# Optimization experiments

Measured on AMD Instinct MI355X. Metric: run time of the kernel, lower is better.

The kernel has to match this reference:

```python
import jax, jax.numpy as jnp
import numpy as np

B, S, D, H, G = 16, 512, 1024, 128, 256  # batch, seq, lstm_in, lstm_hidden, gat_dim

def _linear(x, W, b):
    return x @ W.T + b

def _lstm_dir(xs, Wih, Whh, bih, bhh, reverse):
    # xs: [S, B, Din] -> hs: [S, B, H]; PyTorch gate order i, f, g, o
    b = bih + bhh
    def step(carry, xt):
        h, c = carry
        z = xt @ Wih.T + h @ Whh.T + b
        i, f, g, o = jnp.split(z, 4, axis=-1)
        c = jax.nn.sigmoid(f) * c + jax.nn.sigmoid(i) * jnp.tanh(g)
        h = jax.nn.sigmoid(o) * jnp.tanh(c)
        return (h, c), h
    init = (jnp.zeros((xs.shape[1], Whh.shape[1]), xs.dtype),
            jnp.zeros((xs.shape[1], Whh.shape[1]), xs.dtype))
    _, hs = jax.lax.scan(step, init, xs, reverse=reverse)
    return hs

def _forward(x, adj,
             l0f_Wih, l0f_Whh, l0f_bih, l0f_bhh, l0b_Wih, l0b_Whh, l0b_bih, l0b_bhh,
             l1f_Wih, l1f_Whh, l1f_bih, l1f_bhh, l1b_Wih, l1b_Whh, l1b_bih, l1b_bhh,
             fc1_W, fc1_b, wattn_W, wattn_b, lin0_W, lin0_b, lin1_W, lin1_b,
             linf_W, linf_b, fcA_W, fcA_b, fcB_W, fcB_b, fcC_W, fcC_b):
    # ---- 2-layer bidirectional LSTM ----
    xs = jnp.swapaxes(x, 0, 1)  # [S, B, D]
    h0 = jnp.concatenate([_lstm_dir(xs, l0f_Wih, l0f_Whh, l0f_bih, l0f_bhh, False),
                          _lstm_dir(xs, l0b_Wih, l0b_Whh, l0b_bih, l0b_bhh, True)], axis=-1)
    h1 = jnp.concatenate([_lstm_dir(h0, l1f_Wih, l1f_Whh, l1f_bih, l1f_bhh, False),
                          _lstm_dir(h0, l1b_Wih, l1b_Whh, l1b_bih, l1b_bhh, True)], axis=-1)
    out_lstm = jnp.swapaxes(h1, 0, 1)  # [B, S, 2H]
    # ---- GAT on fc1(x) ----
    g = _linear(x, fc1_W, fc1_b)  # [B, S, G]
    idx = jnp.arange(S)
    adj = adj.at[:, idx, idx].set(1.0)
    eye = 1e-05 * jnp.eye(S, dtype=x.dtype)
    for l in range(4):
        g0 = g
        q = _linear(g, wattn_W[l], wattn_b[l])
        a = jax.nn.sigmoid(jnp.einsum('bij,bkj->bik', q, g)) + eye
        a = a * adj
        a = a / jnp.sum(a, axis=2, keepdims=True)
        g = jnp.einsum('bij,bjd->bid', a, g)
        g = jax.nn.relu(_linear(g, lin0_W[l], lin0_b[l]))
        g = jax.nn.relu(_linear(g, lin1_W[l], lin1_b[l]))
        g = g + g0
    g = _linear(g, linf_W, linf_b)
    # ---- head (dropout in eval mode -> identity) ----
    hidden = jnp.mean(jnp.concatenate([out_lstm, g], axis=2), axis=1)  # [B, 512]
    y = jax.nn.leaky_relu(_linear(hidden, fcA_W, fcA_b), 0.1)
    y = jax.nn.leaky_relu(_linear(y, fcB_W, fcB_b), 0.1)
    y = _linear(y, fcC_W, fcC_b)  # [B, 2]
    return y, hidden


def setup_inputs() -> dict:
    key = jax.random.key(0)
    ks = jax.random.split(key, 40)
    r = lambda k, shape: jax.random.normal(k, shape, jnp.float32) * 0.05
    inp = {}
    inp['x'] = jax.random.normal(ks[0], (B, S, D), jnp.float32)
    inp['adj'] = (jax.random.uniform(ks[1], (B, S, S)) < 0.05).astype(jnp.float32)
    # LSTM params: layer0 input D, layer1 input 2H; forward/backward directions
    inp['l0f_Wih'] = r(ks[2], (4 * H, D)); inp['l0f_Whh'] = r(ks[3], (4 * H, H))
    inp['l0f_bih'] = r(ks[4], (4 * H,));  inp['l0f_bhh'] = r(ks[5], (4 * H,))
    inp['l0b_Wih'] = r(ks[6], (4 * H, D)); inp['l0b_Whh'] = r(ks[7], (4 * H, H))
    inp['l0b_bih'] = r(ks[8], (4 * H,));  inp['l0b_bhh'] = r(ks[9], (4 * H,))
    inp['l1f_Wih'] = r(ks[10], (4 * H, 2 * H)); inp['l1f_Whh'] = r(ks[11], (4 * H, H))
    inp['l1f_bih'] = r(ks[12], (4 * H,)); inp['l1f_bhh'] = r(ks[13], (4 * H,))
    inp['l1b_Wih'] = r(ks[14], (4 * H, 2 * H)); inp['l1b_Whh'] = r(ks[15], (4 * H, H))
    inp['l1b_bih'] = r(ks[16], (4 * H,)); inp['l1b_bhh'] = r(ks[17], (4 * H,))
    inp['fc1_W'] = r(ks[18], (G, D)); inp['fc1_b'] = r(ks[19], (G,))
    inp['wattn_W'] = r(ks[20], (4, G, G)); inp['wattn_b'] = r(ks[21], (4, G))
    inp['lin0_W'] = r(ks[22], (4, G, G)); inp['lin0_b'] = r(ks[23], (4, G))
    inp['lin1_W'] = r(ks[24], (4, G, G)); inp['lin1_b'] = r(ks[25], (4, G))
    inp['linf_W'] = r(ks[26], (G, G)); inp['linf_b'] = r(ks[27], (G,))
    inp['fcA_W'] = r(ks[28], (128, 512)); inp['fcA_b'] = r(ks[29], (128,))
    inp['fcB_W'] = r(ks[30], (32, 128)); inp['fcB_b'] = r(ks[31], (32,))
    inp['fcC_W'] = r(ks[32], (2, 32)); inp['fcC_b'] = r(ks[33], (2,))
    return inp


def reference(x, adj,
              l0f_Wih, l0f_Whh, l0f_bih, l0f_bhh, l0b_Wih, l0b_Whh, l0b_bih, l0b_bhh,
              l1f_Wih, l1f_Whh, l1f_bih, l1f_bhh, l1b_Wih, l1b_Whh, l1b_bih, l1b_bhh,
              fc1_W, fc1_b, wattn_W, wattn_b, lin0_W, lin0_b, lin1_W, lin1_b,
              linf_W, linf_b, fcA_W, fcA_b, fcB_W, fcB_b, fcC_W, fcC_b):
    return _forward(x, adj,
                    l0f_Wih, l0f_Whh, l0f_bih, l0f_bhh, l0b_Wih, l0b_Whh, l0b_bih, l0b_bhh,
                    l1f_Wih, l1f_Whh, l1f_bih, l1f_bhh, l1b_Wih, l1b_Whh, l1b_bih, l1b_bhh,
                    fc1_W, fc1_b, wattn_W, wattn_b, lin0_W, lin0_b, lin1_W, lin1_b,
                    linf_W, linf_b, fcA_W, fcA_b, fcB_W, fcB_b, fcC_W, fcC_b)
```

## Files before the change

kernel.cpp:

```cpp
#include <hip/hip_runtime.h>
#include <stdint.h>

#define B_ 16
#define S_ 512
#define D_ 1024
#define H4 512
#define G_ 256

typedef unsigned short u16;
using short8 = __attribute__((ext_vector_type(8))) short;
using f32x4  = __attribute__((ext_vector_type(4))) float;

__device__ __forceinline__ u16 f2bf(float f){
  unsigned int u = __float_as_uint(f);
  u += 0x7fffu + ((u >> 16) & 1u);
  return (u16)(u >> 16);
}
__device__ __forceinline__ float bf2f(u16 h){
  return __uint_as_float(((unsigned int)h) << 16);
}

struct CvtSegs {
  const float4* src[14];
  short4* dst[14];
  int blk0[15];
};
__global__ __launch_bounds__(256) void cvt_multi(CvtSegs cs){
  int blk = blockIdx.x;
  int s = 0;
  #pragma unroll
  for (int k = 0; k < 14; ++k) if (cs.blk0[k + 1] <= blk) s = k + 1;
  int i = (blk - cs.blk0[s]) * 256 + threadIdx.x;
  float4 v = cs.src[s][i];
  short4 o;
  o.x = (short)f2bf(v.x); o.y = (short)f2bf(v.y);
  o.z = (short)f2bf(v.z); o.w = (short)f2bf(v.w);
  cs.dst[s][i] = o;
}

__global__ __launch_bounds__(256) void bias_prep(const float* a,const float* b,const float* c,const float* d,
                                                 const float* e,const float* f,const float* g,const float* h,
                                                 float* out){
  int i = blockIdx.x * 256 + threadIdx.x;
  if (i >= 2048) return;
  int p = i >> 9, k = i & 511;
  const float* x1 = (p==0)?a:(p==1)?c:(p==2)?e:g;
  const float* x2 = (p==0)?b:(p==1)?d:(p==2)?f:h;
  out[i] = x1[k] + x2[k];
}

template<int EPI, bool OUT_BF16, int PERM, bool RESID>
__device__ __forceinline__ void gemm_bt_body(
    const u16* __restrict__ A, const u16* __restrict__ W,
    const float* __restrict__ bias, const u16* __restrict__ resid,
    const float* __restrict__ ex,
    void* __restrict__ outp, int M, int N, int K,
    long sA, long sW, long sO, int bx, int by, int bz)
{
  const u16* Ab = A + (long)bz * sA;
  const u16* Wb = W + (long)bz * sW;
  const int bm0 = by * 64, bn0 = bx * 64;
  const int tid = threadIdx.x;
  const int l = tid & 63, wid = tid >> 6;
  const int wm = (wid >> 1) * 32, wn = (wid & 1) * 32;
  const int lr = l & 15, lk8 = (l >> 4) * 8;

  const f32x4 z4 = {0.f, 0.f, 0.f, 0.f};
  f32x4 acc[2][2] = {{z4, z4}, {z4, z4}};

  const u16* Ap0 = Ab + (long)(bm0 + wm + lr) * K + lk8;
  const u16* Wp0 = Wb + (long)(bn0 + wn + lr) * K + lk8;
  for (int k0 = 0; k0 < K; k0 += 32) {
    short8 a0 = *reinterpret_cast<const short8*>(Ap0 + k0);
    short8 a1 = *reinterpret_cast<const short8*>(Ap0 + (long)16 * K + k0);
    short8 b0 = *reinterpret_cast<const short8*>(Wp0 + k0);
    short8 b1 = *reinterpret_cast<const short8*>(Wp0 + (long)16 * K + k0);
    acc[0][0] = __builtin_amdgcn_mfma_f32_16x16x32_bf16(a0, b0, acc[0][0], 0, 0, 0);
    acc[0][1] = __builtin_amdgcn_mfma_f32_16x16x32_bf16(a0, b1, acc[0][1], 0, 0, 0);
    acc[1][0] = __builtin_amdgcn_mfma_f32_16x16x32_bf16(a1, b0, acc[1][0], 0, 0, 0);
    acc[1][1] = __builtin_amdgcn_mfma_f32_16x16x32_bf16(a1, b1, acc[1][1], 0, 0, 0);
  }
  #pragma unroll
  for (int mt = 0; mt < 2; ++mt)
  #pragma unroll
  for (int nt = 0; nt < 2; ++nt) {
    int n = bn0 + wn + 16 * nt + lr;
    float bv = bias ? bias[n] : 0.f;
    #pragma unroll
    for (int r = 0; r < 4; ++r) {
      int m = bm0 + wm + 16 * mt + (l >> 4) * 4 + r;
      float v = acc[mt][nt][r] + bv;
      if (EPI == 1) v = fmaxf(v, 0.f);
      if (EPI == 2) {
        float sg = __fdividef(1.f, 1.f + __expf(-v));
        v = (n == m) ? (sg + 1e-5f) : sg * ex[((long)bz * 512 + m) * 512 + n];
      }
      if (EPI == 3) v *= ex[(long)bz * 512 + m];
      if (RESID) v += bf2f(resid[(long)m * N + n]);
      long oi;
      if (PERM == 2) {
        int t = m & 511, b = m >> 9;
        oi = (long)((t * 16 + b) * 128 + (n & 127)) * 4 + (n >> 7);
      } else {
        oi = (long)bz * sO + (long)m * N + n;
      }
      if (OUT_BF16) ((u16*)outp)[oi] = f2bf(v);
      else          ((float*)outp)[oi] = v;
    }
  }
}

template<int EPI, bool OUT_BF16, int PERM, bool RESID>
__global__ __launch_bounds__(256) void gemm_bt(
    const u16* __restrict__ A, const u16* __restrict__ W,
    const float* __restrict__ bias, const u16* __restrict__ resid,
    const float* __restrict__ ex,
    void* __restrict__ outp, int M, int N, int K,
    long sA, long sW, long sO)
{
  gemm_bt_body<EPI, OUT_BF16, PERM, RESID>(A, W, bias, resid, ex, outp, M, N, K,
                                           sA, sW, sO, blockIdx.x, blockIdx.y, blockIdx.z);
}

__global__ __launch_bounds__(256) void proj2(
    const u16* __restrict__ A, const u16* __restrict__ W0, const u16* __restrict__ W1,
    const float* __restrict__ bias, float* __restrict__ O0, float* __restrict__ O1, int K)
{
  int z = blockIdx.z;
  gemm_bt_body<0, false, 2, false>(A, z ? W1 : W0, bias + z * 512, nullptr, nullptr,
                                   z ? O1 : O0, 8192, 512, K, 0, 0, 0,
                                   blockIdx.x, blockIdx.y, 0);
}

__device__ __forceinline__ void gemm_bt_body8(
    const u16* __restrict__ A, const u16* __restrict__ W,
    const float* __restrict__ bias, u16* __restrict__ out,
    int N, int K, int bx, int by)
{
  const int bm0 = by * 64, bn0 = bx * 128;
  const int tid = threadIdx.x;
  const int l = tid & 63, wid = tid >> 6;
  const int wm = (wid >> 2) * 32, wn = (wid & 3) * 32;
  const int lr = l & 15, lk8 = (l >> 4) * 8;

  const f32x4 z4 = {0.f, 0.f, 0.f, 0.f};
  f32x4 acc[2][2] = {{z4, z4}, {z4, z4}};

  const u16* Ap0 = A + (long)(bm0 + wm + lr) * K + lk8;
  const u16* Wp0 = W + (long)(bn0 + wn + lr) * K + lk8;
  for (int k0 = 0; k0 < K; k0 += 32) {
    short8 a0 = *reinterpret_cast<const short8*>(Ap0 + k0);
    short8 a1 = *reinterpret_cast<const short8*>(Ap0 + (long)16 * K + k0);
    short8 b0 = *reinterpret_cast<const short8*>(Wp0 + k0);
    short8 b1 = *reinterpret_cast<const short8*>(Wp0 + (long)16 * K + k0);
    acc[0][0] = __builtin_amdgcn_mfma_f32_16x16x32_bf16(a0, b0, acc[0][0], 0, 0, 0);
    acc[0][1] = __builtin_amdgcn_mfma_f32_16x16x32_bf16(a0, b1, acc[0][1], 0, 0, 0);
    acc[1][0] = __builtin_amdgcn_mfma_f32_16x16x32_bf16(a1, b0, acc[1][0], 0, 0, 0);
    acc[1][1] = __builtin_amdgcn_mfma_f32_16x16x32_bf16(a1, b1, acc[1][1], 0, 0, 0);
  }
  #pragma unroll
  for (int mt = 0; mt < 2; ++mt)
  #pragma unroll
  for (int nt = 0; nt < 2; ++nt) {
    int n = bn0 + wn + 16 * nt + lr;
    float bv = bias[n];
    #pragma unroll
    for (int r = 0; r < 4; ++r) {
      int m = bm0 + wm + 16 * mt + (l >> 4) * 4 + r;
      out[(long)m * N + n] = f2bf(acc[mt][nt][r] + bv);
    }
  }
}

__device__ __forceinline__ void lstm_scan9_body(
    const float* __restrict__ X, const u16* __restrict__ Whh,
    u16* __restrict__ Hout, int dir, int bat0)
{
  __shared__ __align__(16) u16 hbuf[2][16][136];

  const int tid = threadIdx.x;
  const int l = tid & 63, w = tid >> 6;
  const int lr = l & 15, lk = l >> 4;

  short8 bfrag[4][4];
  #pragma unroll
  for (int g = 0; g < 4; ++g)
    #pragma unroll
    for (int ks = 0; ks < 4; ++ks)
      bfrag[g][ks] = *reinterpret_cast<const short8*>(
          Whh + (g * 128 + 16 * w + lr) * 128 + 32 * ks + 8 * lk);

  for (int i = tid; i < 2 * 16 * 136; i += 512) ((u16*)hbuf)[i] = 0;

  float c = 0.f;
  const f32x4 z4 = {0.f, 0.f, 0.f, 0.f};

  auto ldX = [&](int t) -> float4 {
    int ta = dir ? (S_ - 1 - t) : t;
    return *reinterpret_cast<const float4*>(
        X + (size_t)((ta * 16 + bat0 + lk) * 128 + 16 * w + lr) * 4);
  };
  float4 xA = ldX(0), xB = ldX(1), xC = ldX(2), xD;
  __syncthreads();

  auto step = [&](int t, float4& xc, float4& xt, int tload) {
    const int p = t & 1;
    short8 af[4];
    #pragma unroll
    for (int ks = 0; ks < 4; ++ks)
      af[ks] = *reinterpret_cast<const short8*>(&hbuf[p][lr][32 * ks + 8 * lk]);
    f32x4 acc[4] = {z4, z4, z4, z4};
    #pragma unroll
    for (int g = 0; g < 4; ++g)
      #pragma unroll
      for (int ks = 0; ks < 4; ++ks)
        acc[g] = __builtin_amdgcn_mfma_f32_16x16x32_bf16(af[ks], bfrag[g][ks], acc[g], 0, 0, 0);
    if (tload < S_) xt = ldX(tload);
    float zi = acc[0][0] + xc.x;
    float zf = acc[1][0] + xc.y;
    float zg = acc[2][0] + xc.z;
    float zo = acc[3][0] + xc.w;
    float si = __fdividef(1.f, 1.f + __expf(-zi));
    float sf = __fdividef(1.f, 1.f + __expf(-zf));
    float so = __fdividef(1.f, 1.f + __expf(-zo));
    float eg = __expf(2.f * zg);
    float tg = 1.f - __fdividef(2.f, eg + 1.f);
    c = sf * c + si * tg;
    float ec = __expf(2.f * c);
    float tc = 1.f - __fdividef(2.f, ec + 1.f);
    u16 hb = f2bf(so * tc);
    int ta = dir ? (S_ - 1 - t) : t;
    hbuf[p ^ 1][4 * lk][16 * w + lr] = hb;
    Hout[((size_t)(bat0 + lk) * S_ + ta) * 256 + dir * 128 + 16 * w + lr] = hb;
    asm volatile("s_waitcnt lgkmcnt(0)" ::: "memory");
    __builtin_amdgcn_s_barrier();
  };

  for (int t = 0; t < S_; t += 4) {
    step(t,     xA, xD, t + 3);
    step(t + 1, xB, xA, t + 4);
    step(t + 2, xC, xB, t + 5);
    step(t + 3, xD, xC, t + 6);
  }
}

__global__ __launch_bounds__(512, 1) void scan_fused(
    const float* __restrict__ Xf, const float* __restrict__ Xb,
    const u16* __restrict__ Whhf, const u16* __restrict__ Whhb,
    u16* __restrict__ Hout,
    const u16* __restrict__ gA, const u16* __restrict__ gW,
    const float* __restrict__ gb, u16* __restrict__ gOut, int gK)
{
  if (blockIdx.x < 8) {
    int dir = blockIdx.x & 1, bat0 = (blockIdx.x >> 1) * 4;
    lstm_scan9_body(dir ? Xb : Xf, dir ? Whhb : Whhf, Hout, dir, bat0);
  } else {
    int bi = blockIdx.x - 8;
    gemm_bt_body8(gA, gW, gb, gOut, 256, gK, bi & 1, bi >> 1);
  }
}

__device__ __forceinline__ void transpose_body(const u16* __restrict__ in, u16* __restrict__ out,
                                               int bz, int s0, int d0)
{
  __shared__ u16 tile[32][33];
  int tx = threadIdx.x & 31, ty = threadIdx.x >> 5;
  const u16* ip = in + (long)bz * 512 * 256;
  u16* op = out + (long)bz * 256 * 512;
  #pragma unroll
  for (int k = 0; k < 32; k += 8) tile[ty + k][tx] = ip[(long)(s0 + ty + k) * 256 + d0 + tx];
  __syncthreads();
  #pragma unroll
  for (int k = 0; k < 32; k += 8) op[(long)(d0 + ty + k) * 512 + s0 + tx] = tile[tx][ty + k];
}

__global__ __launch_bounds__(256) void transpose_g(const u16* __restrict__ in, u16* __restrict__ out)
{
  transpose_body(in, out, blockIdx.z, blockIdx.x * 32, blockIdx.y * 32);
}

__global__ __launch_bounds__(256) void wattn_trans(
    const u16* __restrict__ gcur, const u16* __restrict__ wW, const float* __restrict__ wb,
    u16* __restrict__ qb, u16* __restrict__ gT)
{
  if (blockIdx.x < 512) {
    int b = blockIdx.x;
    gemm_bt_body<0, true, 0, false>(gcur, wW, wb, nullptr, nullptr, qb,
                                    8192, 256, 256, 0, 0, 0, b & 3, b >> 2, 0);
  } else {
    int b = blockIdx.x - 512;
    int bz = b >> 7, rem = b & 127;
    transpose_body(gcur, gT, bz, (rem & 15) * 32, (rem >> 4) * 32);
  }
}

__global__ __launch_bounds__(256) void rowsum_inv(const u16* __restrict__ abf, float* __restrict__ rinv)
{
  int bz = blockIdx.y;
  int row = blockIdx.x * 4 + (threadIdx.x >> 6);
  int l = threadIdx.x & 63;
  short8 v = *reinterpret_cast<const short8*>(abf + ((size_t)bz * 512 + row) * 512 + l * 8);
  float s = 0.f;
  #pragma unroll
  for (int k = 0; k < 8; ++k) s += bf2f((u16)v[k]);
  #pragma unroll
  for (int off = 32; off; off >>= 1) s += __shfl_xor(s, off);
  if (l == 0) rinv[bz * 512 + row] = __fdividef(1.f, s);
}

__global__ __launch_bounds__(256) void mean_cat(
    const u16* __restrict__ lstm, const u16* __restrict__ gf, float* __restrict__ dout)
{
  int b = blockIdx.x;
  for (int cc = threadIdx.x; cc < 512; cc += 256) {
    const u16* src = (cc < 256) ? (lstm + (long)b * 512 * 256 + cc)
                                : (gf   + (long)b * 512 * 256 + (cc - 256));
    float s = 0.f;
    for (int t = 0; t < 512; ++t) s += bf2f(src[(long)t * 256]);
    dout[32 + b * 512 + cc] = s * (1.f / 512.f);
  }
}

__global__ __launch_bounds__(256) void head_kernel(
    const float* __restrict__ hidden,
    const float* __restrict__ fcA_W, const float* __restrict__ fcA_b,
    const float* __restrict__ fcB_W, const float* __restrict__ fcB_b,
    const float* __restrict__ fcC_W, const float* __restrict__ fcC_b,
    float* __restrict__ y)
{
  __shared__ float hb[16 * 512];
  __shared__ float ab[16 * 128];
  __shared__ float bb[16 * 32];
  int tid = threadIdx.x;
  for (int i = tid; i < 8192; i += 256) hb[i] = hidden[i];
  __syncthreads();
  for (int o = tid; o < 2048; o += 256) {
    int b = o >> 7, jj = o & 127;
    float acc = fcA_b[jj];
    const float* wrow = fcA_W + jj * 512;
    const float* hrow = hb + b * 512;
    for (int k = 0; k < 512; ++k) acc += hrow[k] * wrow[k];
    ab[o] = acc > 0.f ? acc : 0.1f * acc;
  }
  __syncthreads();
  for (int o = tid; o < 512; o += 256) {
    int b = o >> 5, jj = o & 31;
    float acc = fcB_b[jj];
    for (int k = 0; k < 128; ++k) acc += ab[b * 128 + k] * fcB_W[jj * 128 + k];
    bb[o] = acc > 0.f ? acc : 0.1f * acc;
  }
  __syncthreads();
  if (tid < 32) {
    int b = tid >> 1, jj = tid & 1;
    float acc = fcC_b[jj];
    for (int k = 0; k < 32; ++k) acc += bb[b * 32 + k] * fcC_W[jj * 32 + k];
    y[b * 2 + jj] = acc;
  }
}

extern "C" void kernel_launch(void* const* d_in, const int* in_sizes, int n_in,
                              void* d_out, int out_size, void* d_ws, size_t ws_size,
                              hipStream_t stream)
{
  const float* x       = (const float*)d_in[0];
  const float* adj     = (const float*)d_in[1];
  const float* l0f_Wih = (const float*)d_in[2];
  const float* l0f_Whh = (const float*)d_in[3];
  const float* l0f_bih = (const float*)d_in[4];
  const float* l0f_bhh = (const float*)d_in[5];
  const float* l0b_Wih = (const float*)d_in[6];
  const float* l0b_Whh = (const float*)d_in[7];
  const float* l0b_bih = (const float*)d_in[8];
  const float* l0b_bhh = (const float*)d_in[9];
  const float* l1f_Wih = (const float*)d_in[10];
  const float* l1f_Whh = (const float*)d_in[11];
  const float* l1f_bih = (const float*)d_in[12];
  const float* l1f_bhh = (const float*)d_in[13];
  const float* l1b_Wih = (const float*)d_in[14];
  const float* l1b_Whh = (const float*)d_in[15];
  const float* l1b_bih = (const float*)d_in[16];
  const float* l1b_bhh = (const float*)d_in[17];
  const float* fc1_W   = (const float*)d_in[18];
  const float* fc1_b   = (const float*)d_in[19];
  const float* wattn_W = (const float*)d_in[20];
  const float* wattn_b = (const float*)d_in[21];
  const float* lin0_W  = (const float*)d_in[22];
  const float* lin0_b  = (const float*)d_in[23];
  const float* lin1_W  = (const float*)d_in[24];
  const float* lin1_b  = (const float*)d_in[25];
  const float* linf_W  = (const float*)d_in[26];
  const float* linf_b  = (const float*)d_in[27];
  const float* fcA_W   = (const float*)d_in[28];
  const float* fcA_b   = (const float*)d_in[29];
  const float* fcB_W   = (const float*)d_in[30];
  const float* fcB_b   = (const float*)d_in[31];
  const float* fcC_W   = (const float*)d_in[32];
  const float* fcC_b   = (const float*)d_in[33];

  char* wp = (char*)d_ws;
  auto alloc = [&](size_t n) -> void* { void* p = wp; wp += (n + 255) & ~(size_t)255; return p; };

  u16* x_bf     = (u16*)alloc((size_t)B_ * S_ * D_ * 2);
  u16* w0f_ih   = (u16*)alloc((size_t)512 * 1024 * 2);
  u16* w0b_ih   = (u16*)alloc((size_t)512 * 1024 * 2);
  u16* w1f_ih   = (u16*)alloc((size_t)512 * 256 * 2);
  u16* w1b_ih   = (u16*)alloc((size_t)512 * 256 * 2);
  u16* w0f_hh   = (u16*)alloc((size_t)512 * 128 * 2);
  u16* w0b_hh   = (u16*)alloc((size_t)512 * 128 * 2);
  u16* w1f_hh   = (u16*)alloc((size_t)512 * 128 * 2);
  u16* w1b_hh   = (u16*)alloc((size_t)512 * 128 * 2);
  u16* wfc1     = (u16*)alloc((size_t)256 * 1024 * 2);
  u16* wattn_bf = (u16*)alloc((size_t)4 * 256 * 256 * 2);
  u16* wlin0_bf = (u16*)alloc((size_t)4 * 256 * 256 * 2);
  u16* wlin1_bf = (u16*)alloc((size_t)4 * 256 * 256 * 2);
  u16* wlinf_bf = (u16*)alloc((size_t)256 * 256 * 2);
  float* bias4  = (float*)alloc((size_t)2048 * 4);
  float* X0f    = (float*)alloc((size_t)S_ * 16 * 512 * 4);
  float* X0b    = (float*)alloc((size_t)S_ * 16 * 512 * 4);
  u16* h0       = (u16*)alloc((size_t)B_ * S_ * 256 * 2);
  u16* lstm_out = (u16*)alloc((size_t)B_ * S_ * 256 * 2);
  u16* gA       = (u16*)alloc((size_t)B_ * S_ * 256 * 2);
  u16* gB       = (u16*)alloc((size_t)B_ * S_ * 256 * 2);
  u16* qb       = (u16*)alloc((size_t)B_ * S_ * 256 * 2);
  u16* gT       = (u16*)alloc((size_t)B_ * S_ * 256 * 2);
  u16* t1       = (u16*)alloc((size_t)B_ * S_ * 256 * 2);
  u16* t2       = (u16*)alloc((size_t)B_ * S_ * 256 * 2);
  u16* abf      = (u16*)alloc((size_t)B_ * S_ * S_ * 2);
  float* rinv   = (float*)alloc((size_t)B_ * S_ * 4);

  CvtSegs cs;
  int nb = 0, si = 0;
  auto seg = [&](const float* s, u16* d, int n) {
    cs.src[si] = (const float4*)s; cs.dst[si] = (short4*)d;
    cs.blk0[si] = nb; nb += (n / 4 + 255) / 256; ++si;
  };
  seg(x, x_bf, B_ * S_ * D_);
  seg(l0f_Wih, w0f_ih, 512 * 1024);
  seg(l0b_Wih, w0b_ih, 512 * 1024);
  seg(l1f_Wih, w1f_ih, 512 * 256);
  seg(l1b_Wih, w1b_ih, 512 * 256);
  seg(l0f_Whh, w0f_hh, 512 * 128);
  seg(l0b_Whh, w0b_hh, 512 * 128);
  seg(l1f_Whh, w1f_hh, 512 * 128);
  seg(l1b_Whh, w1b_hh, 512 * 128);
  seg(fc1_W, wfc1, 256 * 1024);
  seg(wattn_W, wattn_bf, 4 * 256 * 256);
  seg(lin0_W, wlin0_bf, 4 * 256 * 256);
  seg(lin1_W, wlin1_bf, 4 * 256 * 256);
  seg(linf_W, wlinf_bf, 256 * 256);
  for (int k = si; k <= 14; ++k) cs.blk0[k] = nb;
  cvt_multi<<<nb, 256, 0, stream>>>(cs);
  bias_prep<<<8, 256, 0, stream>>>(l0f_bih, l0f_bhh, l0b_bih, l0b_bhh,
                                   l1f_bih, l1f_bhh, l1b_bih, l1b_bhh, bias4);

  proj2<<<dim3(8, 128, 2), 256, 0, stream>>>(x_bf, w0f_ih, w0b_ih, bias4, X0f, X0b, 1024);
  scan_fused<<<8 + 256, 512, 0, stream>>>(X0f, X0b, w0f_hh, w0b_hh, h0,
                                          x_bf, wfc1, fc1_b, gA, 1024);
  proj2<<<dim3(8, 128, 2), 256, 0, stream>>>(h0, w1f_ih, w1b_ih, bias4 + 1024, X0f, X0b, 256);
  scan_fused<<<8 + 256, 512, 0, stream>>>(X0f, X0b, w1f_hh, w1b_hh, lstm_out,
                                          gA, wattn_bf, wattn_b, qb, 256);

  u16* gcur = gA; u16* gnext = gB;
  for (int lyr = 0; lyr < 4; ++lyr) {
    if (lyr == 0)
      transpose_g<<<dim3(16, 8, 16), 256, 0, stream>>>(gcur, gT);
    else
      wattn_trans<<<512 + 2048, 256, 0, stream>>>(gcur, wattn_bf + lyr * 65536,
                                                  wattn_b + lyr * 256, qb, gT);
    gemm_bt<2, true, 0, false><<<dim3(8, 8, 16), 256, 0, stream>>>(
        qb, gcur, nullptr, nullptr, adj, abf, 512, 512, 256, 131072, 131072, 262144);
    rowsum_inv<<<dim3(128, 16), 256, 0, stream>>>(abf, rinv);
    gemm_bt<3, true, 0, false><<<dim3(4, 8, 16), 256, 0, stream>>>(
        abf, gT, nullptr, nullptr, rinv, t1, 512, 256, 512, 262144, 131072, 131072);
    gemm_bt<1, true, 0, false><<<dim3(4, 128, 1), 256, 0, stream>>>(
        t1, wlin0_bf + lyr * 65536, lin0_b + lyr * 256, nullptr, nullptr, t2, 8192, 256, 256, 0, 0, 0);
    gemm_bt<1, true, 0, true><<<dim3(4, 128, 1), 256, 0, stream>>>(
        t2, wlin1_bf + lyr * 65536, lin1_b + lyr * 256, gcur, nullptr, gnext, 8192, 256, 256, 0, 0, 0);
    u16* tmp = gcur; gcur = gnext; gnext = tmp;
  }
  gemm_bt<0, true, 0, false><<<dim3(4, 128, 1), 256, 0, stream>>>(
      gcur, wlinf_bf, linf_b, nullptr, nullptr, t2, 8192, 256, 256, 0, 0, 0);

  mean_cat<<<16, 256, 0, stream>>>(lstm_out, t2, (float*)d_out);
  head_kernel<<<1, 256, 0, stream>>>((const float*)d_out + 32,
                                     fcA_W, fcA_b, fcB_W, fcB_b, fcC_W, fcC_b,
                                     (float*)d_out);
}
```

Baseline: 1.225 ms.

## Run full GAT pipeline inside LSTM scan kernels with global-flag grid barriers

Moves the whole GAT stack (fc1, all four attention layers, and the final linear) into the two persistent scan kernels. Blocks beyond the eight LSTM blocks execute GAT stages, separated by atomic-counter grid barriers, so the GAT work overlaps the latency-bound recurrent scans instead of running as a chain of separate launches afterward. Each 512-thread block is treated as two virtual 256-thread workers. The risk is deadlock if the 264 blocks cannot all be resident at once, plus the cost of spin barriers. mean_cat is also rewritten so each thread sums one lstm column and one GAT column with coalesced reads.

```diff
diff --git a/kernel.cpp b/kernel.cpp
--- a/kernel.cpp
+++ b/kernel.cpp
@@ -55,12 +55,11 @@
     const float* __restrict__ bias, const u16* __restrict__ resid,
     const float* __restrict__ ex,
     void* __restrict__ outp, int M, int N, int K,
-    long sA, long sW, long sO, int bx, int by, int bz)
+    long sA, long sW, long sO, int bx, int by, int bz, int tid)
 {
   const u16* Ab = A + (long)bz * sA;
   const u16* Wb = W + (long)bz * sW;
   const int bm0 = by * 64, bn0 = bx * 64;
-  const int tid = threadIdx.x;
   const int l = tid & 63, wid = tid >> 6;
   const int wm = (wid >> 1) * 32, wn = (wid & 1) * 32;
   const int lr = l & 15, lk8 = (l >> 4) * 8;
@@ -110,18 +109,6 @@
   }
 }
 
-template<int EPI, bool OUT_BF16, int PERM, bool RESID>
-__global__ __launch_bounds__(256) void gemm_bt(
-    const u16* __restrict__ A, const u16* __restrict__ W,
-    const float* __restrict__ bias, const u16* __restrict__ resid,
-    const float* __restrict__ ex,
-    void* __restrict__ outp, int M, int N, int K,
-    long sA, long sW, long sO)
-{
-  gemm_bt_body<EPI, OUT_BF16, PERM, RESID>(A, W, bias, resid, ex, outp, M, N, K,
-                                           sA, sW, sO, blockIdx.x, blockIdx.y, blockIdx.z);
-}
-
 __global__ __launch_bounds__(256) void proj2(
     const u16* __restrict__ A, const u16* __restrict__ W0, const u16* __restrict__ W1,
     const float* __restrict__ bias, float* __restrict__ O0, float* __restrict__ O1, int K)
@@ -129,47 +116,36 @@
   int z = blockIdx.z;
   gemm_bt_body<0, false, 2, false>(A, z ? W1 : W0, bias + z * 512, nullptr, nullptr,
                                    z ? O1 : O0, 8192, 512, K, 0, 0, 0,
-                                   blockIdx.x, blockIdx.y, 0);
-}
-
-__device__ __forceinline__ void gemm_bt_body8(
-    const u16* __restrict__ A, const u16* __restrict__ W,
-    const float* __restrict__ bias, u16* __restrict__ out,
-    int N, int K, int bx, int by)
-{
-  const int bm0 = by * 64, bn0 = bx * 128;
-  const int tid = threadIdx.x;
-  const int l = tid & 63, wid = tid >> 6;
-  const int wm = (wid >> 2) * 32, wn = (wid & 3) * 32;
-  const int lr = l & 15, lk8 = (l >> 4) * 8;
-
-  const f32x4 z4 = {0.f, 0.f, 0.f, 0.f};
-  f32x4 acc[2][2] = {{z4, z4}, {z4, z4}};
-
-  const u16* Ap0 = A + (long)(bm0 + wm + lr) * K + lk8;
-  const u16* Wp0 = W + (long)(bn0 + wn + lr) * K + lk8;
-  for (int k0 = 0; k0 < K; k0 += 32) {
-    short8 a0 = *reinterpret_cast<const short8*>(Ap0 + k0);
-    short8 a1 = *reinterpret_cast<const short8*>(Ap0 + (long)16 * K + k0);
-    short8 b0 = *reinterpret_cast<const short8*>(Wp0 + k0);
-    short8 b1 = *reinterpret_cast<const short8*>(Wp0 + (long)16 * K + k0);
-    acc[0][0] = __builtin_amdgcn_mfma_f32_16x16x32_bf16(a0, b0, acc[0][0], 0, 0, 0);
-    acc[0][1] = __builtin_amdgcn_mfma_f32_16x16x32_bf16(a0, b1, acc[0][1], 0, 0, 0);
-    acc[1][0] = __builtin_amdgcn_mfma_f32_16x16x32_bf16(a1, b0, acc[1][0], 0, 0, 0);
-    acc[1][1] = __builtin_amdgcn_mfma_f32_16x16x32_bf16(a1, b1, acc[1][1], 0, 0, 0);
-  }
-  #pragma unroll
-  for (int mt = 0; mt < 2; ++mt)
-  #pragma unroll
-  for (int nt = 0; nt < 2; ++nt) {
-    int n = bn0 + wn + 16 * nt + lr;
-    float bv = bias[n];
-    #pragma unroll
-    for (int r = 0; r < 4; ++r) {
-      int m = bm0 + wm + 16 * mt + (l >> 4) * 4 + r;
-      out[(long)m * N + n] = f2bf(acc[mt][nt][r] + bv);
-    }
-  }
+                                   blockIdx.x, blockIdx.y, 0, threadIdx.x);
+}
+
+__device__ __forceinline__ void transpose_body(const u16* __restrict__ in, u16* __restrict__ out,
+                                               int bz, int s0, int d0, int tid,
+                                               u16 (*tile)[33])
+{
+  int tx = tid & 31, ty = (tid >> 5) & 7;
+  const u16* ip = in + (long)bz * 512 * 256;
+  u16* op = out + (long)bz * 256 * 512;
+  #pragma unroll
+  for (int k = 0; k < 32; k += 8) tile[ty + k][tx] = ip[(long)(s0 + ty + k) * 256 + d0 + tx];
+  __syncthreads();
+  #pragma unroll
+  for (int k = 0; k < 32; k += 8) op[(long)(d0 + ty + k) * 512 + s0 + tx] = tile[tx][ty + k];
+  __syncthreads();
+}
+
+__device__ __forceinline__ void rowsum_body(const u16* __restrict__ abf, float* __restrict__ rinv,
+                                            int bx, int bz, int tid)
+{
+  int row = bx * 4 + ((tid >> 6) & 3);
+  int l = tid & 63;
+  short8 v = *reinterpret_cast<const short8*>(abf + ((size_t)bz * 512 + row) * 512 + l * 8);
+  float s = 0.f;
+  #pragma unroll
+  for (int k = 0; k < 8; ++k) s += bf2f((u16)v[k]);
+  #pragma unroll
+  for (int off = 32; off; off >>= 1) s += __shfl_xor(s, off);
+  if (l == 0) rinv[bz * 512 + row] = __fdividef(1.f, s);
 }
 
 __device__ __forceinline__ void lstm_scan9_body(
@@ -244,81 +220,119 @@
   }
 }
 
-__global__ __launch_bounds__(512, 1) void scan_fused(
+struct GatArgs {
+  const u16 *xbf, *wfc1;
+  const float *fc1b;
+  const u16 *wattn; const float *wattnb;
+  const u16 *wlin0; const float *lin0b;
+  const u16 *wlin1; const float *lin1b;
+  const u16 *wlinf; const float *linfb;
+  const float *adj;
+  u16 *gA, *gB, *qb, *gT, *t1, *t2, *abf;
+  float *rinv;
+  unsigned *flags;
+};
+
+__device__ __forceinline__ void gat_part(const GatArgs& a, int wid, int W, int part,
+                                         u16 (*myTile)[33])
+{
+  const int half = threadIdx.x >> 8;
+  const int vw = wid * 2 + half;
+  const int tid = threadIdx.x & 255;
+  unsigned* F = a.flags + part * 16;
+  int s = 0;
+
+  auto sync_stage = [&]() {
+    __syncthreads();
+    __threadfence();
+    if (threadIdx.x == 0) {
+      __hip_atomic_fetch_add(F + s, 1u, __ATOMIC_RELEASE, __HIP_MEMORY_SCOPE_AGENT);
+      while (__hip_atomic_load(F + s, __ATOMIC_ACQUIRE, __HIP_MEMORY_SCOPE_AGENT) < (unsigned)W)
+        __builtin_amdgcn_s_sleep(2);
+    }
+    __syncthreads();
+    __threadfence();
+    ++s;
+  };
+
+  if (part == 0) {
+    gemm_bt_body<0, true, 0, false>(a.xbf, a.wfc1, a.fc1b, nullptr, nullptr, a.gA,
+                                    8192, 256, 1024, 0, 0, 0, vw & 3, vw >> 2, 0, tid);
+    sync_stage();
+  }
+
+  for (int l = part * 2; l < part * 2 + 2; ++l) {
+    const u16* in = (l & 1) ? a.gB : a.gA;
+    u16* out      = (l & 1) ? a.gA : a.gB;
+    gemm_bt_body<0, true, 0, false>(in, a.wattn + l * 65536, a.wattnb + l * 256,
+                                    nullptr, nullptr, a.qb,
+                                    8192, 256, 256, 0, 0, 0, vw & 3, vw >> 2, 0, tid);
+    #pragma unroll
+    for (int i = 0; i < 4; ++i) {
+      int t = vw + i * 512;
+      int bz = t >> 7, rem = t & 127;
+      transpose_body(in, a.gT, bz, (rem & 15) * 32, (rem >> 4) * 32, tid, myTile);
+    }
+    sync_stage();
+    #pragma unroll
+    for (int i = 0; i < 2; ++i) {
+      int t = vw + i * 512;
+      gemm_bt_body<2, true, 0, false>(a.qb, in, nullptr, nullptr, a.adj, a.abf,
+                                      512, 512, 256, 131072, 131072, 262144,
+                                      t & 7, (t >> 3) & 7, t >> 6, tid);
+    }
+    sync_stage();
+    #pragma unroll
+    for (int i = 0; i < 4; ++i) {
+      int t = vw + i * 512;
+      rowsum_body(a.abf, a.rinv, t & 127, t >> 7, tid);
+    }
+    sync_stage();
+    gemm_bt_body<3, true, 0, false>(a.abf, a.gT, nullptr, nullptr, a.rinv, a.t1,
+                                    512, 256, 512, 262144, 131072, 131072,
+                                    vw & 3, (vw >> 2) & 7, vw >> 5, tid);
+    sync_stage();
+    gemm_bt_body<1, true, 0, false>(a.t1, a.wlin0 + l * 65536, a.lin0b + l * 256,
+                                    nullptr, nullptr, a.t2,
+                                    8192, 256, 256, 0, 0, 0, vw & 3, vw >> 2, 0, tid);
+    sync_stage();
+    gemm_bt_body<1, true, 0, true>(a.t2, a.wlin1 + l * 65536, a.lin1b + l * 256,
+                                   in, nullptr, out,
+                                   8192, 256, 256, 0, 0, 0, vw & 3, vw >> 2, 0, tid);
+    sync_stage();
+  }
+
+  if (part == 1) {
+    gemm_bt_body<0, true, 0, false>(a.gA, a.wlinf, a.linfb, nullptr, nullptr, a.t2,
+                                    8192, 256, 256, 0, 0, 0, vw & 3, vw >> 2, 0, tid);
+  }
+}
+
+__global__ __launch_bounds__(512, 1) void scan_gat(
     const float* __restrict__ Xf, const float* __restrict__ Xb,
     const u16* __restrict__ Whhf, const u16* __restrict__ Whhb,
-    u16* __restrict__ Hout,
-    const u16* __restrict__ gA, const u16* __restrict__ gW,
-    const float* __restrict__ gb, u16* __restrict__ gOut, int gK)
+    u16* __restrict__ Hout, GatArgs ga, int part, int W)
 {
   if (blockIdx.x < 8) {
     int dir = blockIdx.x & 1, bat0 = (blockIdx.x >> 1) * 4;
     lstm_scan9_body(dir ? Xb : Xf, dir ? Whhb : Whhf, Hout, dir, bat0);
   } else {
-    int bi = blockIdx.x - 8;
-    gemm_bt_body8(gA, gW, gb, gOut, 256, gK, bi & 1, bi >> 1);
-  }
-}
-
-__device__ __forceinline__ void transpose_body(const u16* __restrict__ in, u16* __restrict__ out,
-                                               int bz, int s0, int d0)
-{
-  __shared__ u16 tile[32][33];
-  int tx = threadIdx.x & 31, ty = threadIdx.x >> 5;
-  const u16* ip = in + (long)bz * 512 * 256;
-  u16* op = out + (long)bz * 256 * 512;
-  #pragma unroll
-  for (int k = 0; k < 32; k += 8) tile[ty + k][tx] = ip[(long)(s0 + ty + k) * 256 + d0 + tx];
-  __syncthreads();
-  #pragma unroll
-  for (int k = 0; k < 32; k += 8) op[(long)(d0 + ty + k) * 512 + s0 + tx] = tile[tx][ty + k];
-}
-
-__global__ __launch_bounds__(256) void transpose_g(const u16* __restrict__ in, u16* __restrict__ out)
-{
-  transpose_body(in, out, blockIdx.z, blockIdx.x * 32, blockIdx.y * 32);
-}
-
-__global__ __launch_bounds__(256) void wattn_trans(
-    const u16* __restrict__ gcur, const u16* __restrict__ wW, const float* __restrict__ wb,
-    u16* __restrict__ qb, u16* __restrict__ gT)
-{
-  if (blockIdx.x < 512) {
-    int b = blockIdx.x;
-    gemm_bt_body<0, true, 0, false>(gcur, wW, wb, nullptr, nullptr, qb,
-                                    8192, 256, 256, 0, 0, 0, b & 3, b >> 2, 0);
-  } else {
-    int b = blockIdx.x - 512;
-    int bz = b >> 7, rem = b & 127;
-    transpose_body(gcur, gT, bz, (rem & 15) * 32, (rem >> 4) * 32);
-  }
-}
-
-__global__ __launch_bounds__(256) void rowsum_inv(const u16* __restrict__ abf, float* __restrict__ rinv)
-{
-  int bz = blockIdx.y;
-  int row = blockIdx.x * 4 + (threadIdx.x >> 6);
-  int l = threadIdx.x & 63;
-  short8 v = *reinterpret_cast<const short8*>(abf + ((size_t)bz * 512 + row) * 512 + l * 8);
-  float s = 0.f;
-  #pragma unroll
-  for (int k = 0; k < 8; ++k) s += bf2f((u16)v[k]);
-  #pragma unroll
-  for (int off = 32; off; off >>= 1) s += __shfl_xor(s, off);
-  if (l == 0) rinv[bz * 512 + row] = __fdividef(1.f, s);
+    __shared__ __align__(16) u16 tiles[2][32][33];
+    gat_part(ga, blockIdx.x - 8, W, part, tiles[threadIdx.x >> 8]);
+  }
 }
 
 __global__ __launch_bounds__(256) void mean_cat(
     const u16* __restrict__ lstm, const u16* __restrict__ gf, float* __restrict__ dout)
 {
-  int b = blockIdx.x;
-  for (int cc = threadIdx.x; cc < 512; cc += 256) {
-    const u16* src = (cc < 256) ? (lstm + (long)b * 512 * 256 + cc)
-                                : (gf   + (long)b * 512 * 256 + (cc - 256));
-    float s = 0.f;
-    for (int t = 0; t < 512; ++t) s += bf2f(src[(long)t * 256]);
-    dout[32 + b * 512 + cc] = s * (1.f / 512.f);
-  }
+  int b = blockIdx.x, tid = threadIdx.x;
+  float sl = 0.f, sg = 0.f;
+  for (int t = 0; t < 512; ++t) {
+    sl += bf2f(lstm[((size_t)b * 512 + t) * 256 + tid]);
+    sg += bf2f(gf[((size_t)b * 512 + t) * 256 + tid]);
+  }
+  dout[32 + b * 512 + tid]       = sl * (1.f / 512.f);
+  dout[32 + b * 512 + 256 + tid] = sg * (1.f / 512.f);
 }
 
 __global__ __launch_bounds__(256) void head_kernel(
@@ -400,6 +414,7 @@
   char* wp = (char*)d_ws;
   auto alloc = [&](size_t n) -> void* { void* p = wp; wp += (n + 255) & ~(size_t)255; return p; };
 
+  unsigned* flags = (unsigned*)alloc(256);
   u16* x_bf     = (u16*)alloc((size_t)B_ * S_ * D_ * 2);
   u16* w0f_ih   = (u16*)alloc((size_t)512 * 1024 * 2);
   u16* w0b_ih   = (u16*)alloc((size_t)512 * 1024 * 2);
@@ -428,6 +443,8 @@
   u16* abf      = (u16*)alloc((size_t)B_ * S_ * S_ * 2);
   float* rinv   = (float*)alloc((size_t)B_ * S_ * 4);
 
+  hipMemsetAsync(flags, 0, 256, stream);
+
   CvtSegs cs;
   int nb = 0, si = 0;
   auto seg = [&](const float* s, u16* d, int n) {
@@ -453,33 +470,23 @@
   bias_prep<<<8, 256, 0, stream>>>(l0f_bih, l0f_bhh, l0b_bih, l0b_bhh,
                                    l1f_bih, l1f_bhh, l1b_bih, l1b_bhh, bias4);
 
+  GatArgs ga;
+  ga.xbf = x_bf; ga.wfc1 = wfc1; ga.fc1b = fc1_b;
+  ga.wattn = wattn_bf; ga.wattnb = wattn_b;
+  ga.wlin0 = wlin0_bf; ga.lin0b = lin0_b;
+  ga.wlin1 = wlin1_bf; ga.lin1b = lin1_b;
+  ga.wlinf = wlinf_bf; ga.linfb = linf_b;
+  ga.adj = adj;
+  ga.gA = gA; ga.gB = gB; ga.qb = qb; ga.gT = gT;
+  ga.t1 = t1; ga.t2 = t2; ga.abf = abf; ga.rinv = rinv;
+  ga.flags = flags;
+
+  const int W = 256;
+
   proj2<<<dim3(8, 128, 2), 256, 0, stream>>>(x_bf, w0f_ih, w0b_ih, bias4, X0f, X0b, 1024);
-  scan_fused<<<8 + 256, 512, 0, stream>>>(X0f, X0b, w0f_hh, w0b_hh, h0,
-                                          x_bf, wfc1, fc1_b, gA, 1024);
+  scan_gat<<<8 + W, 512, 0, stream>>>(X0f, X0b, w0f_hh, w0b_hh, h0, ga, 0, W);
   proj2<<<dim3(8, 128, 2), 256, 0, stream>>>(h0, w1f_ih, w1b_ih, bias4 + 1024, X0f, X0b, 256);
-  scan_fused<<<8 + 256, 512, 0, stream>>>(X0f, X0b, w1f_hh, w1b_hh, lstm_out,
-                                          gA, wattn_bf, wattn_b, qb, 256);
-
-  u16* gcur = gA; u16* gnext = gB;
-  for (int lyr = 0; lyr < 4; ++lyr) {
-    if (lyr == 0)
-      transpose_g<<<dim3(16, 8, 16), 256, 0, stream>>>(gcur, gT);
-    else
-      wattn_trans<<<512 + 2048, 256, 0, stream>>>(gcur, wattn_bf + lyr * 65536,
-                                                  wattn_b + lyr * 256, qb, gT);
-    gemm_bt<2, true, 0, false><<<dim3(8, 8, 16), 256, 0, stream>>>(
-        qb, gcur, nullptr, nullptr, adj, abf, 512, 512, 256, 131072, 131072, 262144);
-    rowsum_inv<<<dim3(128, 16), 256, 0, stream>>>(abf, rinv);
-    gemm_bt<3, true, 0, false><<<dim3(4, 8, 16), 256, 0, stream>>>(
-        abf, gT, nullptr, nullptr, rinv, t1, 512, 256, 512, 262144, 131072, 131072);
-    gemm_bt<1, true, 0, false><<<dim3(4, 128, 1), 256, 0, stream>>>(
-        t1, wlin0_bf + lyr * 65536, lin0_b + lyr * 256, nullptr, nullptr, t2, 8192, 256, 256, 0, 0, 0);
-    gemm_bt<1, true, 0, true><<<dim3(4, 128, 1), 256, 0, stream>>>(
-        t2, wlin1_bf + lyr * 65536, lin1_b + lyr * 256, gcur, nullptr, gnext, 8192, 256, 256, 0, 0, 0);
-    u16* tmp = gcur; gcur = gnext; gnext = tmp;
-  }
-  gemm_bt<0, true, 0, false><<<dim3(4, 128, 1), 256, 0, stream>>>(
-      gcur, wlinf_bf, linf_b, nullptr, nullptr, t2, 8192, 256, 256, 0, 0, 0);
+  scan_gat<<<8 + W, 512, 0, stream>>>(X0f, X0b, w1f_hh, w1b_hh, lstm_out, ga, 1, W);
 
   mean_cat<<<16, 256, 0, stream>>>(lstm_out, t2, (float*)d_out);
   head_kernel<<<1, 256, 0, stream>>>((const float*)d_out + 32,
```

New measurement: 4.133 ms. 3.37x slower.

## Interleave forward and backward LSTM directions within one scan block

Applied to the files above, without the earlier changes.

Each scan block now runs both the forward and backward recurrences for its four-batch slice, interleaving their MFMA chains and gate math so the two independent dependency chains can hide each other's latency. This halves the number of scan blocks and keeps both directions' recurrent weights in registers, which raises register pressure. The per-step barrier is shared by both directions. Separately, mean_cat is rewritten so each thread reduces one LSTM column and one GAT column in a single loop, giving coalesced reads.

```diff
diff --git a/kernel.cpp b/kernel.cpp
--- a/kernel.cpp
+++ b/kernel.cpp
@@ -55,12 +55,11 @@
     const float* __restrict__ bias, const u16* __restrict__ resid,
     const float* __restrict__ ex,
     void* __restrict__ outp, int M, int N, int K,
-    long sA, long sW, long sO, int bx, int by, int bz)
+    long sA, long sW, long sO, int bx, int by, int bz, int tid)
 {
   const u16* Ab = A + (long)bz * sA;
   const u16* Wb = W + (long)bz * sW;
   const int bm0 = by * 64, bn0 = bx * 64;
-  const int tid = threadIdx.x;
   const int l = tid & 63, wid = tid >> 6;
   const int wm = (wid >> 1) * 32, wn = (wid & 1) * 32;
   const int lr = l & 15, lk8 = (l >> 4) * 8;
@@ -119,7 +118,8 @@
     long sA, long sW, long sO)
 {
   gemm_bt_body<EPI, OUT_BF16, PERM, RESID>(A, W, bias, resid, ex, outp, M, N, K,
-                                           sA, sW, sO, blockIdx.x, blockIdx.y, blockIdx.z);
+                                           sA, sW, sO, blockIdx.x, blockIdx.y, blockIdx.z,
+                                           threadIdx.x);
 }
 
 __global__ __launch_bounds__(256) void proj2(
@@ -129,7 +129,7 @@
   int z = blockIdx.z;
   gemm_bt_body<0, false, 2, false>(A, z ? W1 : W0, bias + z * 512, nullptr, nullptr,
                                    z ? O1 : O0, 8192, 512, K, 0, 0, 0,
-                                   blockIdx.x, blockIdx.y, 0);
+                                   blockIdx.x, blockIdx.y, 0, threadIdx.x);
 }
 
 __device__ __forceinline__ void gemm_bt_body8(
@@ -172,50 +172,44 @@
   }
 }
 
-__device__ __forceinline__ void lstm_scan9_body(
-    const float* __restrict__ X, const u16* __restrict__ Whh,
-    u16* __restrict__ Hout, int dir, int bat0)
-{
-  __shared__ __align__(16) u16 hbuf[2][16][136];
+__device__ __forceinline__ void lstm_scan10_body(
+    const float* __restrict__ Xf, const float* __restrict__ Xb,
+    const u16* __restrict__ Whhf, const u16* __restrict__ Whhb,
+    u16* __restrict__ Hout, int bat0)
+{
+  __shared__ __align__(16) u16 hbuf[2][2][16][136];
 
   const int tid = threadIdx.x;
   const int l = tid & 63, w = tid >> 6;
   const int lr = l & 15, lk = l >> 4;
 
-  short8 bfrag[4][4];
+  short8 wf[2][4][4];
   #pragma unroll
   for (int g = 0; g < 4; ++g)
     #pragma unroll
-    for (int ks = 0; ks < 4; ++ks)
-      bfrag[g][ks] = *reinterpret_cast<const short8*>(
-          Whh + (g * 128 + 16 * w + lr) * 128 + 32 * ks + 8 * lk);
-
-  for (int i = tid; i < 2 * 16 * 136; i += 512) ((u16*)hbuf)[i] = 0;
-
-  float c = 0.f;
+    for (int ks = 0; ks < 4; ++ks) {
+      wf[0][g][ks] = *reinterpret_cast<const short8*>(
+          Whhf + (g * 128 + 16 * w + lr) * 128 + 32 * ks + 8 * lk);
+      wf[1][g][ks] = *reinterpret_cast<const short8*>(
+          Whhb + (g * 128 + 16 * w + lr) * 128 + 32 * ks + 8 * lk);
+    }
+
+  for (int i = tid; i < 2 * 2 * 16 * 136; i += 512) ((u16*)hbuf)[i] = 0;
+
+  float c0 = 0.f, c1 = 0.f;
   const f32x4 z4 = {0.f, 0.f, 0.f, 0.f};
 
-  auto ldX = [&](int t) -> float4 {
-    int ta = dir ? (S_ - 1 - t) : t;
+  auto ldX = [&](int d, int t) -> float4 {
+    int ta = d ? (S_ - 1 - t) : t;
+    const float* X = d ? Xb : Xf;
     return *reinterpret_cast<const float4*>(
         X + (size_t)((ta * 16 + bat0 + lk) * 128 + 16 * w + lr) * 4);
   };
-  float4 xA = ldX(0), xB = ldX(1), xC = ldX(2), xD;
+  float4 a0 = ldX(0, 0), a1 = ldX(0, 1), a2 = ldX(0, 2), a3;
+  float4 b0 = ldX(1, 0), b1 = ldX(1, 1), b2 = ldX(1, 2), b3;
   __syncthreads();
 
-  auto step = [&](int t, float4& xc, float4& xt, int tload) {
-    const int p = t & 1;
-    short8 af[4];
-    #pragma unroll
-    for (int ks = 0; ks < 4; ++ks)
-      af[ks] = *reinterpret_cast<const short8*>(&hbuf[p][lr][32 * ks + 8 * lk]);
-    f32x4 acc[4] = {z4, z4, z4, z4};
-    #pragma unroll
-    for (int g = 0; g < 4; ++g)
-      #pragma unroll
-      for (int ks = 0; ks < 4; ++ks)
-        acc[g] = __builtin_amdgcn_mfma_f32_16x16x32_bf16(af[ks], bfrag[g][ks], acc[g], 0, 0, 0);
-    if (tload < S_) xt = ldX(tload);
+  auto gates = [&](const f32x4 (&acc)[4], const float4& xc, float& c, int d, int t) {
     float zi = acc[0][0] + xc.x;
     float zf = acc[1][0] + xc.y;
     float zg = acc[2][0] + xc.z;
@@ -229,18 +223,40 @@
     float ec = __expf(2.f * c);
     float tc = 1.f - __fdividef(2.f, ec + 1.f);
     u16 hb = f2bf(so * tc);
-    int ta = dir ? (S_ - 1 - t) : t;
-    hbuf[p ^ 1][4 * lk][16 * w + lr] = hb;
-    Hout[((size_t)(bat0 + lk) * S_ + ta) * 256 + dir * 128 + 16 * w + lr] = hb;
+    int ta = d ? (S_ - 1 - t) : t;
+    hbuf[d][(t & 1) ^ 1][4 * lk][16 * w + lr] = hb;
+    Hout[((size_t)(bat0 + lk) * S_ + ta) * 256 + d * 128 + 16 * w + lr] = hb;
+  };
+
+  auto step = [&](int t, float4& xc0, float4& xt0, float4& xc1, float4& xt1, int tload) {
+    const int p = t & 1;
+    short8 af0[4], af1[4];
+    #pragma unroll
+    for (int ks = 0; ks < 4; ++ks) {
+      af0[ks] = *reinterpret_cast<const short8*>(&hbuf[0][p][lr][32 * ks + 8 * lk]);
+      af1[ks] = *reinterpret_cast<const short8*>(&hbuf[1][p][lr][32 * ks + 8 * lk]);
+    }
+    f32x4 acc0[4] = {z4, z4, z4, z4};
+    f32x4 acc1[4] = {z4, z4, z4, z4};
+    #pragma unroll
+    for (int g = 0; g < 4; ++g)
+      #pragma unroll
+      for (int ks = 0; ks < 4; ++ks) {
+        acc0[g] = __builtin_amdgcn_mfma_f32_16x16x32_bf16(af0[ks], wf[0][g][ks], acc0[g], 0, 0, 0);
+        acc1[g] = __builtin_amdgcn_mfma_f32_16x16x32_bf16(af1[ks], wf[1][g][ks], acc1[g], 0, 0, 0);
+      }
+    if (tload < S_) { xt0 = ldX(0, tload); xt1 = ldX(1, tload); }
+    gates(acc0, xc0, c0, 0, t);
+    gates(acc1, xc1, c1, 1, t);
     asm volatile("s_waitcnt lgkmcnt(0)" ::: "memory");
     __builtin_amdgcn_s_barrier();
   };
 
   for (int t = 0; t < S_; t += 4) {
-    step(t,     xA, xD, t + 3);
-    step(t + 1, xB, xA, t + 4);
-    step(t + 2, xC, xB, t + 5);
-    step(t + 3, xD, xC, t + 6);
+    step(t,     a0, a3, b0, b3, t + 3);
+    step(t + 1, a1, a0, b1, b0, t + 4);
+    step(t + 2, a2, a1, b2, b1, t + 5);
+    step(t + 3, a3, a2, b3, b2, t + 6);
   }
 }
 
@@ -251,11 +267,10 @@
     const u16* __restrict__ gA, const u16* __restrict__ gW,
     const float* __restrict__ gb, u16* __restrict__ gOut, int gK)
 {
-  if (blockIdx.x < 8) {
-    int dir = blockIdx.x & 1, bat0 = (blockIdx.x >> 1) * 4;
-    lstm_scan9_body(dir ? Xb : Xf, dir ? Whhb : Whhf, Hout, dir, bat0);
+  if (blockIdx.x < 4) {
+    lstm_scan10_body(Xf, Xb, Whhf, Whhb, Hout, blockIdx.x * 4);
   } else {
-    int bi = blockIdx.x - 8;
+    int bi = blockIdx.x - 4;
     gemm_bt_body8(gA, gW, gb, gOut, 256, gK, bi & 1, bi >> 1);
   }
 }
@@ -286,7 +301,7 @@
   if (blockIdx.x < 512) {
     int b = blockIdx.x;
     gemm_bt_body<0, true, 0, false>(gcur, wW, wb, nullptr, nullptr, qb,
-                                    8192, 256, 256, 0, 0, 0, b & 3, b >> 2, 0);
+                                    8192, 256, 256, 0, 0, 0, b & 3, b >> 2, 0, threadIdx.x);
   } else {
     int b = blockIdx.x - 512;
     int bz = b >> 7, rem = b & 127;
@@ -311,14 +326,14 @@
 __global__ __launch_bounds__(256) void mean_cat(
     const u16* __restrict__ lstm, const u16* __restrict__ gf, float* __restrict__ dout)
 {
-  int b = blockIdx.x;
-  for (int cc = threadIdx.x; cc < 512; cc += 256) {
-    const u16* src = (cc < 256) ? (lstm + (long)b * 512 * 256 + cc)
-                                : (gf   + (long)b * 512 * 256 + (cc - 256));
-    float s = 0.f;
-    for (int t = 0; t < 512; ++t) s += bf2f(src[(long)t * 256]);
-    dout[32 + b * 512 + cc] = s * (1.f / 512.f);
-  }
+  int b = blockIdx.x, tid = threadIdx.x;
+  float sl = 0.f, sg = 0.f;
+  for (int t = 0; t < 512; ++t) {
+    sl += bf2f(lstm[((size_t)b * 512 + t) * 256 + tid]);
+    sg += bf2f(gf[((size_t)b * 512 + t) * 256 + tid]);
+  }
+  dout[32 + b * 512 + tid]       = sl * (1.f / 512.f);
+  dout[32 + b * 512 + 256 + tid] = sg * (1.f / 512.f);
 }
 
 __global__ __launch_bounds__(256) void head_kernel(
@@ -454,10 +469,10 @@
                                    l1f_bih, l1f_bhh, l1b_bih, l1b_bhh, bias4);
 
   proj2<<<dim3(8, 128, 2), 256, 0, stream>>>(x_bf, w0f_ih, w0b_ih, bias4, X0f, X0b, 1024);
-  scan_fused<<<8 + 256, 512, 0, stream>>>(X0f, X0b, w0f_hh, w0b_hh, h0,
+  scan_fused<<<4 + 256, 512, 0, stream>>>(X0f, X0b, w0f_hh, w0b_hh, h0,
                                           x_bf, wfc1, fc1_b, gA, 1024);
   proj2<<<dim3(8, 128, 2), 256, 0, stream>>>(h0, w1f_ih, w1b_ih, bias4 + 1024, X0f, X0b, 256);
-  scan_fused<<<8 + 256, 512, 0, stream>>>(X0f, X0b, w1f_hh, w1b_hh, lstm_out,
+  scan_fused<<<4 + 256, 512, 0, stream>>>(X0f, X0b, w1f_hh, w1b_hh, lstm_out,
                                           gA, wattn_bf, wattn_b, qb, 256);
 
   u16* gcur = gA; u16* gnext = gB;
```

Result: slower. 1.763 ms (+43.9%).
